# Optimization experiments

Measured on AMD Instinct MI355X. Metric: run time of the kernel, lower is better.

Reference implementation:

```python
import jax, jax.numpy as jnp
import numpy as np

D_MODEL = 1024
NUM_HEADS = 16
D_QK = D_MODEL // NUM_HEADS  # 64
SEQ_LEN = 4096
BATCH = 1
ROPE_THETA = 10000.0


def _apply_rope(x, positions):
    # x: [B, H, S, d], positions: [1, 1, S]
    d = x.shape[-1]
    inv_freq = 1.0 / (ROPE_THETA ** (jnp.arange(0, d, 2, dtype=jnp.float32) / d))  # [d/2]
    ang = positions.astype(jnp.float32)[..., None] * inv_freq  # [1,1,S,d/2]
    cos, sin = jnp.cos(ang), jnp.sin(ang)
    x1, x2 = x[..., 0::2], x[..., 1::2]
    out_even = x1 * cos - x2 * sin
    out_odd = x1 * sin + x2 * cos
    return jnp.stack([out_even, out_odd], axis=-1).reshape(x.shape)


def setup_inputs() -> dict:
    key = jax.random.key(0)
    ks = jax.random.split(key, 9)
    s = 1.0 / np.sqrt(D_MODEL)
    return {
        "x": jax.random.normal(ks[0], (BATCH, SEQ_LEN, D_MODEL), dtype=jnp.float32),
        "Wq": jax.random.normal(ks[1], (D_MODEL, D_MODEL), dtype=jnp.float32) * s,
        "bq": jnp.zeros((D_MODEL,), dtype=jnp.float32),
        "Wk": jax.random.normal(ks[2], (D_MODEL, D_MODEL), dtype=jnp.float32) * s,
        "bk": jnp.zeros((D_MODEL,), dtype=jnp.float32),
        "Wv": jax.random.normal(ks[3], (D_MODEL, D_MODEL), dtype=jnp.float32) * s,
        "bv": jnp.zeros((D_MODEL,), dtype=jnp.float32),
        "Wo": jax.random.normal(ks[4], (D_MODEL, D_MODEL), dtype=jnp.float32) * s,
        "bo": jnp.zeros((D_MODEL,), dtype=jnp.float32),
    }


def reference(x, Wq, bq, Wk, bk, Wv, bv, Wo, bo):
    B, S, D = x.shape
    H, dk = NUM_HEADS, D_QK
    positions = jnp.arange(S).reshape(1, 1, S)
    # torch Linear: x @ W.T + b. NOTE: original reshapes (B,S,H*dk) -> (B,H,S,dk)
    # without a transpose; we reproduce that exact (quirky) reshape.
    q = (x @ Wq.T + bq).reshape(B, H, S, dk)
    k = (x @ Wk.T + bk).reshape(B, H, S, dk)
    v = (x @ Wv.T + bv).reshape(B, H, S, dk)
    q = _apply_rope(q, positions)
    k = _apply_rope(k, positions)
    scores = jnp.einsum('bhqd,bhkd->bhqk', q, k) / jnp.sqrt(jnp.float32(dk))
    mask = jnp.tril(jnp.ones((S, S), dtype=bool))
    scores = jnp.where(mask, scores, -jnp.inf)
    attn = jax.nn.softmax(scores, axis=-1)
    out = jnp.einsum('bhqk,bhkd->bhqd', attn, v)  # [B,H,S,dk]
    concat = out.reshape(B, S, H * dk)  # mirrors original reshape back
    return concat @ Wo.T + bo
```

## Files before the change

kernel.cpp:

```cpp
#include <hip/hip_runtime.h>
#include <hip/hip_bf16.h>

typedef float f32x4 __attribute__((ext_vector_type(4)));
typedef __bf16 bf16x8 __attribute__((ext_vector_type(8)));
typedef short s16x4 __attribute__((ext_vector_type(4)));
typedef unsigned int u32;
typedef unsigned int u32x2 __attribute__((ext_vector_type(2)));
typedef unsigned short u16;

#define SEQ   4096
#define DM    1024
#define HEADS 16
#define DH    64

#if __has_builtin(__builtin_amdgcn_mfma_f32_16x16x16bf16_1k)
#define MFMA16_1K(A, B, C) __builtin_amdgcn_mfma_f32_16x16x16bf16_1k(A, B, C, 0, 0, 0)
#else
#define MFMA16_1K(A, B, C) (C)
#endif
#if __has_builtin(__builtin_amdgcn_exp2f)
#define FEXP2(x) __builtin_amdgcn_exp2f(x)
#else
#define FEXP2(x) exp2f(x)
#endif

__device__ __forceinline__ void async16(void* lds, const void* g) {
  __builtin_amdgcn_global_load_lds((const __attribute__((address_space(1))) u32*)g,
                                   (__attribute__((address_space(3))) u32*)lds, 16, 0, 0);
}

__device__ __forceinline__ u32 lds_addr(const void* p) {
  return (u32)(size_t)(const __attribute__((address_space(3))) char*)p;
}

__device__ __forceinline__ int swz(int row, int off) {
  return row * 128 + (off ^ ((((row >> 3) ^ row) & 7) << 4));
}

__device__ __forceinline__ float ubf2f(u32 u) {
  union { u32 x; float f; } c; c.x = u << 16; return c.f;
}
__device__ __forceinline__ u32 packbf(float a, float b) {
  __hip_bfloat16 ha = __float2bfloat16(a), hb = __float2bfloat16(b);
  return (u32)(*(u16*)&ha) | ((u32)(*(u16*)&hb) << 16);
}

__global__ __launch_bounds__(256) void prep_kernel(
    const float* __restrict__ x,  const float* __restrict__ Wq,
    const float* __restrict__ Wk, const float* __restrict__ Wv,
    const float* __restrict__ Wo, const float* __restrict__ bq,
    const float* __restrict__ bk, const float* __restrict__ bv,
    __hip_bfloat16* __restrict__ xb, __hip_bfloat16* __restrict__ Wqkv,
    __hip_bfloat16* __restrict__ Wob, float* __restrict__ bqkv)
{
  const int NX = SEQ * DM;
  const int NW = DM * DM;
  const int TOT = NX + 4 * NW + 3 * DM;
  for (int idx = blockIdx.x * 256 + threadIdx.x; idx < TOT; idx += gridDim.x * 256) {
    if (idx < NX) {
      xb[idx] = __float2bfloat16(x[idx]);
    } else if (idx < NX + 3 * NW) {
      int j = idx - NX; int m = j >> 20; int r = j & (NW - 1);
      const float* W = (m == 0) ? Wq : ((m == 1) ? Wk : Wv);
      Wqkv[j] = __float2bfloat16(W[r]);
    } else if (idx < NX + 4 * NW) {
      int r = idx - NX - 3 * NW;
      Wob[r] = __float2bfloat16(Wo[r]);
    } else {
      int r = idx - NX - 4 * NW;
      const float* b = (r < DM) ? bq : ((r < 2 * DM) ? bk : bv);
      bqkv[r] = b[r & (DM - 1)];
    }
  }
}

template<bool F32OUT>
__global__ __launch_bounds__(256) void gemm_bt(
    const __hip_bfloat16* __restrict__ A,
    const __hip_bfloat16* __restrict__ B,
    const float* __restrict__ bias,
    void* __restrict__ C,
    int M, int N, int K)
{
  __shared__ __hip_bfloat16 As[2][128 * 32];
  __shared__ __hip_bfloat16 Bs[2][128 * 32];
  const int tid = threadIdx.x;
  const int wid = tid >> 6, lane = tid & 63;
  const int l15 = lane & 15, l4 = lane >> 4;
  const int wr = wid >> 1, wc = wid & 1;
  const int lin = blockIdx.x;
  const int xcd = lin & 7, j = lin >> 3;
  const int bm = ((xcd << 2) | (j & 3)) * 128;
  const int bn = (j >> 2) * 128;

  f32x4 acc[4][4] = {};

  auto stage = [&](int buf, int k0) {
#pragma unroll
    for (int c = 0; c < 2; ++c) {
      int li = c * 256 + tid;
      const __hip_bfloat16* ga = A + (size_t)(bm + (li >> 2)) * K + k0 + (li & 3) * 8;
      async16((char*)(&As[buf][0]) + (c * 256 + wid * 64) * 16, ga);
    }
#pragma unroll
    for (int c = 0; c < 2; ++c) {
      int li = c * 256 + tid;
      const __hip_bfloat16* gb = B + (size_t)(bn + (li >> 2)) * K + k0 + (li & 3) * 8;
      async16((char*)(&Bs[buf][0]) + (c * 256 + wid * 64) * 16, gb);
    }
  };

  stage(0, 0);
  __syncthreads();
  const int nk = K >> 5;
  int cur = 0;
  for (int t = 0; t < nk; ++t) {
    if (t + 1 < nk) stage(cur ^ 1, (t + 1) << 5);
    bf16x8 af[4], bfr[4];
#pragma unroll
    for (int m = 0; m < 4; ++m)
      af[m] = *(const bf16x8*)(&As[cur][(wr * 64 + m * 16 + l15) * 32 + l4 * 8]);
#pragma unroll
    for (int n = 0; n < 4; ++n)
      bfr[n] = *(const bf16x8*)(&Bs[cur][(wc * 64 + n * 16 + l15) * 32 + l4 * 8]);
#pragma unroll
    for (int m = 0; m < 4; ++m)
#pragma unroll
      for (int n = 0; n < 4; ++n)
        acc[m][n] = __builtin_amdgcn_mfma_f32_16x16x32_bf16(af[m], bfr[n], acc[m][n], 0, 0, 0);
    __syncthreads();
    cur ^= 1;
  }

#pragma unroll
  for (int m = 0; m < 4; ++m) {
#pragma unroll
    for (int n = 0; n < 4; ++n) {
#pragma unroll
      for (int i = 0; i < 4; ++i) {
        int row = bm + wr * 64 + m * 16 + l4 * 4 + i;
        int col = bn + wc * 64 + n * 16 + l15;
        float v = acc[m][n][i] + bias[col];
        int mat = col >> 10;
        int cm = col & 1023;
        size_t oidx = ((size_t)mat << 22) + (size_t)row * DM + cm;
        if constexpr (F32OUT) ((float*)C)[oidx] = v;
        else ((__hip_bfloat16*)C)[oidx] = __float2bfloat16(v);
      }
    }
  }
}

__global__ __launch_bounds__(256) void gemm_bt64(
    const __hip_bfloat16* __restrict__ A,
    const __hip_bfloat16* __restrict__ B,
    const float* __restrict__ bias,
    float* __restrict__ C,
    int M, int N, int K)
{
  __shared__ __hip_bfloat16 As[2][64 * 32];
  __shared__ __hip_bfloat16 Bs[2][128 * 32];
  const int tid = threadIdx.x;
  const int wid = tid >> 6, lane = tid & 63;
  const int l15 = lane & 15, l4 = lane >> 4;
  const int lin = blockIdx.x;
  const int xcd = lin & 7, j = lin >> 3;
  const int bm = ((xcd << 3) | (j & 7)) * 64;
  const int bn = (j >> 3) * 128;

  f32x4 acc[4][2] = {};

  auto stage = [&](int buf, int k0) {
    {
      int li = tid;
      const __hip_bfloat16* ga = A + (size_t)(bm + (li >> 2)) * K + k0 + (li & 3) * 8;
      async16((char*)(&As[buf][0]) + (wid * 64) * 16, ga);
    }
#pragma unroll
    for (int c = 0; c < 2; ++c) {
      int li = c * 256 + tid;
      const __hip_bfloat16* gb = B + (size_t)(bn + (li >> 2)) * K + k0 + (li & 3) * 8;
      async16((char*)(&Bs[buf][0]) + (c * 256 + wid * 64) * 16, gb);
    }
  };

  stage(0, 0);
  __syncthreads();
  const int nk = K >> 5;
  int cur = 0;
  for (int t = 0; t < nk; ++t) {
    if (t + 1 < nk) stage(cur ^ 1, (t + 1) << 5);
    bf16x8 af[4], bfr[2];
#pragma unroll
    for (int m = 0; m < 4; ++m)
      af[m] = *(const bf16x8*)(&As[cur][(m * 16 + l15) * 32 + l4 * 8]);
#pragma unroll
    for (int n = 0; n < 2; ++n)
      bfr[n] = *(const bf16x8*)(&Bs[cur][(wid * 32 + n * 16 + l15) * 32 + l4 * 8]);
#pragma unroll
    for (int m = 0; m < 4; ++m)
#pragma unroll
      for (int n = 0; n < 2; ++n)
        acc[m][n] = __builtin_amdgcn_mfma_f32_16x16x32_bf16(af[m], bfr[n], acc[m][n], 0, 0, 0);
    __syncthreads();
    cur ^= 1;
  }

#pragma unroll
  for (int m = 0; m < 4; ++m) {
#pragma unroll
    for (int n = 0; n < 2; ++n) {
#pragma unroll
      for (int i = 0; i < 4; ++i) {
        int row = bm + m * 16 + l4 * 4 + i;
        int col = bn + wid * 32 + n * 16 + l15;
        C[(size_t)row * DM + col] = acc[m][n][i] + bias[col];
      }
    }
  }
}

__global__ __launch_bounds__(256) void rope_kernel(__hip_bfloat16* __restrict__ Q,
                                                   __hip_bfloat16* __restrict__ K)
{
  const int tid = blockIdx.x * 256 + threadIdx.x;
  const int i  = tid & 31;
  const int s2 = (tid >> 5) & (SEQ - 1);
  float inv = FEXP2(-0.41524101186092f * (float)i);
  float ang = (float)s2 * inv;
  float sn = __sinf(ang), cs = __cosf(ang);
  const float QS = 0.125f * 1.44269504088896f;
  size_t off = (size_t)tid * 2;
  u32 qw = *(u32*)(Q + off);
  float q1 = ubf2f(qw & 0xffffu), q2 = ubf2f(qw >> 16);
  *(u32*)(Q + off) = packbf((q1 * cs - q2 * sn) * QS, (q1 * sn + q2 * cs) * QS);
  u32 kw = *(u32*)(K + off);
  float k1 = ubf2f(kw & 0xffffu), k2 = ubf2f(kw >> 16);
  *(u32*)(K + off) = packbf(k1 * cs - k2 * sn, k1 * sn + k2 * cs);
}

__global__ __launch_bounds__(256) void attn_kernel(
    const __hip_bfloat16* __restrict__ Q,
    const __hip_bfloat16* __restrict__ K,
    const __hip_bfloat16* __restrict__ V,
    u16* __restrict__ Opart,
    float* __restrict__ lbuf)
{
  const int lin = blockIdx.x;
  const int pid  = (lin >> 4) & 31;
  const int half = (lin >> 3) & 1;
  const int h    = (lin & 7) | (((lin >> 9) & 1) << 3);
  const int tid = threadIdx.x, wid = tid >> 6, lane = tid & 63;
  const int l15 = lane & 15, l4 = lane >> 4;
  __shared__ __hip_bfloat16 Ks[2][64 * 64];
  __shared__ __hip_bfloat16 Vs[2][64 * 64];

  const size_t hbase = (size_t)h * SEQ * DH;
  const int qa = pid, qb = 63 - pid;
  const int a  = (pid >= 15) ? 16 : (31 - pid);
  const int t0 = half ? a : 0;
  const int t1 = half ? (64 - pid) : a;
  const int ra = qa * 64 + wid * 16, rb = qb * 64 + wid * 16;

  int goffK[2];
#pragma unroll
  for (int c = 0; c < 2; ++c) {
    int rowc = (wid * 2 + c) * 8 + (lane >> 3);
    int fc = ((wid * 2 + c) ^ (lane >> 3)) & 7;
    goffK[c] = rowc * DH + ((lane & 7) ^ fc) * 8;
  }
  int goffV[2];
#pragma unroll
  for (int c = 0; c < 2; ++c) {
    int s = (wid * 2 + c) * 2 + (lane >> 5);
    int g = s >> 2, n = s & 3;
    goffV[c] = (g * 16 + ((lane & 31) >> 1)) * DH + n * 16 + (lane & 1) * 8;
  }

  bf16x8 qfa[2], qfb[2];
#pragma unroll
  for (int dk = 0; dk < 2; ++dk) {
    qfa[dk] = *(const bf16x8*)(Q + hbase + (size_t)(ra + l15) * DH + dk * 32 + l4 * 8);
    qfb[dk] = *(const bf16x8*)(Q + hbase + (size_t)(rb + l15) * DH + dk * 32 + l4 * 8);
  }

  f32x4 oa[4] = {}, ob[4] = {};
  float la = 0.f, lb = 0.f;

  const u32 vsb0 = lds_addr(&Vs[0][0]) + (u32)(l15 * 8 + l4 * 128);
  const u32 vsb1 = vsb0 + 8192;

  auto stageK = [&](int buf, int tt) {
#pragma unroll
    for (int c = 0; c < 2; ++c)
      async16((char*)(&Ks[buf][0]) + (wid * 2 + c) * 1024,
              K + hbase + (size_t)tt * 64 * DH + goffK[c]);
  };
  auto stageV = [&](int buf, int tt) {
#pragma unroll
    for (int c = 0; c < 2; ++c)
      async16((char*)(&Vs[buf][0]) + (wid * 2 + c) * 1024,
              V + hbase + (size_t)tt * 64 * DH + goffV[c]);
  };

#define TRD(dst, base, imm) \
  asm volatile("ds_read_b64_tr_b16 %0, %1 offset:" #imm : "=v"(dst) : "v"(base))
#define CVTPK(d, a, b) \
  asm("v_cvt_pk_bf16_f32 %0, %1, %2" : "=v"(d) : "v"(a), "v"(b))
#define PV4(g) \
  { u32x2 wp_ = { w[g][0], w[g][1] }; \
    s16x4 pa_ = __builtin_bit_cast(s16x4, wp_); \
    _Pragma("unroll") \
    for (int n_ = 0; n_ < 4; ++n_) \
      oacc[n_] = MFMA16_1K(vr[g][n_], pa_, oacc[n_]); }

  auto frag = [&](int buf, int kb, bool diag, const bf16x8* qf, int r0,
                  float& l, f32x4* oacc) {
    const int myq = r0 + l15;
    f32x4 s[4];
#pragma unroll
    for (int g = 0; g < 4; ++g) {
      f32x4 z = {0.f, 0.f, 0.f, 0.f};
#pragma unroll
      for (int dk = 0; dk < 2; ++dk) {
        bf16x8 kf = *(const bf16x8*)((char*)(&Ks[buf][0]) +
                     swz(g * 16 + l15, dk * 64 + l4 * 16));
        z = __builtin_amdgcn_mfma_f32_16x16x32_bf16(kf, qf[dk], z, 0, 0, 0);
      }
      s[g] = z;
    }
    if (diag) {
#pragma unroll
      for (int g = 0; g < 4; ++g)
#pragma unroll
        for (int i = 0; i < 4; ++i)
          if (kb + g * 16 + l4 * 4 + i > myq) s[g][i] = -1e30f;
    }
#pragma unroll
    for (int g = 0; g < 4; ++g)
#pragma unroll
      for (int i = 0; i < 4; ++i) s[g][i] = FEXP2(s[g][i]);
    float rs = 0.f;
#pragma unroll
    for (int g = 0; g < 4; ++g)
      rs += (s[g][0] + s[g][1]) + (s[g][2] + s[g][3]);
    l += rs;
    u32 w[4][2];
#pragma unroll
    for (int g = 0; g < 4; ++g) {
      CVTPK(w[g][0], s[g][0], s[g][1]);
      CVTPK(w[g][1], s[g][2], s[g][3]);
    }
    const u32 va = buf ? vsb1 : vsb0;
    s16x4 vr[4][4];
    TRD(vr[0][0], va, 0);    TRD(vr[0][1], va, 512);
    TRD(vr[0][2], va, 1024); TRD(vr[0][3], va, 1536);
    TRD(vr[1][0], va, 2048); TRD(vr[1][1], va, 2560);
    TRD(vr[1][2], va, 3072); TRD(vr[1][3], va, 3584);
    asm volatile("s_waitcnt lgkmcnt(4)" ::: "memory");
    __builtin_amdgcn_sched_barrier(0);
    TRD(vr[2][0], va, 4096); TRD(vr[2][1], va, 4608);
    TRD(vr[2][2], va, 5120); TRD(vr[2][3], va, 5632);
    PV4(0)
    asm volatile("s_waitcnt lgkmcnt(4)" ::: "memory");
    __builtin_amdgcn_sched_barrier(0);
    TRD(vr[3][0], va, 6144); TRD(vr[3][1], va, 6656);
    TRD(vr[3][2], va, 7168); TRD(vr[3][3], va, 7680);
    PV4(1)
    asm volatile("s_waitcnt lgkmcnt(4)" ::: "memory");
    __builtin_amdgcn_sched_barrier(0);
    PV4(2)
    asm volatile("s_waitcnt lgkmcnt(0)" ::: "memory");
    __builtin_amdgcn_sched_barrier(0);
    PV4(3)
  };

  stageK(0, t0);
  stageV(0, t0);
  __syncthreads();

  for (int t = t0; t < t1; ++t) {
    const int cur = (t - t0) & 1, nxt = cur ^ 1;
    const bool pre = (t + 1 < t1);
    if (pre) { stageK(nxt, t + 1); stageV(nxt, t + 1); }
    frag(cur, t * 64, t == qb, qfb, rb, lb, ob);
    if (t <= qa) frag(cur, t * 64, t == qa, qfa, ra, la, oa);
    __syncthreads();
  }
#undef TRD
#undef CVTPK
#undef PV4

  la += __shfl_xor(la, 16); la += __shfl_xor(la, 32);
  lb += __shfl_xor(lb, 16); lb += __shfl_xor(lb, 32);
  auto write_partial = [&](int qt, float l, f32x4* oacc) {
    float rinv = (l > 0.f) ? 1.0f / l : 0.f;
    const int row = wid * 16 + l15;
    u16* po = Opart + ((((size_t)qt * HEADS + h) * 2 + half) * 64 + row) * 64;
#pragma unroll
    for (int n = 0; n < 4; ++n)
#pragma unroll
      for (int p = 0; p < 2; ++p)
        *(u32*)(po + n * 16 + l4 * 4 + 2 * p) =
            packbf(oacc[n][2 * p] * rinv, oacc[n][2 * p + 1] * rinv);
    if (l4 == 0)
      lbuf[((qt * HEADS + h) * 2 + half) * 64 + row] = l;
  };
  write_partial(qb, lb, ob);
  write_partial(qa, la, oa);
}

__global__ __launch_bounds__(256) void combine_kernel(
    const u16* __restrict__ Opart, const float* __restrict__ lbuf,
    __hip_bfloat16* __restrict__ concat)
{
  const int id = blockIdx.x * 256 + threadIdx.x;
  const int d0 = (id & 7) * 8;
  const int row = (id >> 3) & 63;
  const int h  = (id >> 9) & 15;
  const int qt = id >> 13;
  const int lb0 = ((qt * HEADS + h) * 2) * 64 + row;
  float w0 = lbuf[lb0], w1 = lbuf[lb0 + 64];
  float inv = 1.0f / (w0 + w1);
  w0 *= inv; w1 *= inv;
  size_t ob = (((size_t)(qt * HEADS + h) * 2) * 64 + row) * 64 + d0;
  uint4 a0 = *(const uint4*)(Opart + ob);
  uint4 a1 = *(const uint4*)(Opart + ob + 64 * 64);
  const u16* b0 = (const u16*)&a0; const u16* b1 = (const u16*)&a1;
  u32 outw[4];
#pragma unroll
  for (int j = 0; j < 4; ++j) {
    float e0 = ubf2f(b0[2 * j])     * w0 + ubf2f(b1[2 * j])     * w1;
    float e1 = ubf2f(b0[2 * j + 1]) * w0 + ubf2f(b1[2 * j + 1]) * w1;
    outw[j] = packbf(e0, e1);
  }
  *(uint4*)(concat + (size_t)h * SEQ * DH + (size_t)(qt * 64 + row) * DH + d0) =
      *(const uint4*)outw;
}

extern "C" void kernel_launch(void* const* d_in, const int* in_sizes, int n_in,
                              void* d_out, int out_size, void* d_ws, size_t ws_size,
                              hipStream_t stream) {
  (void)in_sizes; (void)n_in; (void)out_size; (void)ws_size;
  const float* x  = (const float*)d_in[0];
  const float* Wq = (const float*)d_in[1];
  const float* bq = (const float*)d_in[2];
  const float* Wk = (const float*)d_in[3];
  const float* bk = (const float*)d_in[4];
  const float* Wv = (const float*)d_in[5];
  const float* bv = (const float*)d_in[6];
  const float* Wo = (const float*)d_in[7];
  const float* bo = (const float*)d_in[8];

  char* ws = (char*)d_ws;
  __hip_bfloat16* Qbuf   = (__hip_bfloat16*)(ws + 0);
  __hip_bfloat16* Kbuf   = (__hip_bfloat16*)(ws + 8388608);
  __hip_bfloat16* Vbuf   = (__hip_bfloat16*)(ws + 16777216);
  __hip_bfloat16* concat = (__hip_bfloat16*)(ws + 25165824);
  __hip_bfloat16* Wob    = (__hip_bfloat16*)(ws + 33554432);
  float*          bqkv   = (float*)(ws + 35651584);
  float*          lbuf   = (float*)(ws + 35717120);
  __hip_bfloat16* xb     = (__hip_bfloat16*)(ws + 36765696);
  __hip_bfloat16* Wqkv   = (__hip_bfloat16*)(ws + 45154304);
  u16*            Opart  = (u16*)(ws + 36765696);

  prep_kernel<<<2048, 256, 0, stream>>>(x, Wq, Wk, Wv, Wo, bq, bk, bv, xb, Wqkv, Wob, bqkv);
  gemm_bt<false><<<768, 256, 0, stream>>>(xb, Wqkv, bqkv, (void*)Qbuf, SEQ, 3072, DM);
  rope_kernel<<<8192, 256, 0, stream>>>(Qbuf, Kbuf);
  attn_kernel<<<1024, 256, 0, stream>>>(Qbuf, Kbuf, Vbuf, Opart, lbuf);
  combine_kernel<<<2048, 256, 0, stream>>>(Opart, lbuf, concat);
  gemm_bt64<<<512, 256, 0, stream>>>(concat, Wob, bo, (float*)d_out, SEQ, DM, DM);
}
```

Measured before the change: 151.9 us.

## Fuse split-KV partial combine into output projection GEMM A-tile loading

Removes the separate combine kernel and instead merges the two attention partials (weighted by their softmax sums) while loading each A tile in the output-projection GEMM. The concat buffer's write and read round trip and one kernel launch go away. In exchange, the A loads become synchronous global loads with per-element arithmetic inside the GEMM main loop instead of async copies. Because the same A data is recombined for each of the 8 column-tile blocks, the combine arithmetic is repeated, and the loads may stall the pipeline.

```diff
diff --git a/kernel.cpp b/kernel.cpp
--- a/kernel.cpp
+++ b/kernel.cpp
@@ -151,8 +151,9 @@
   }
 }
 
-__global__ __launch_bounds__(256) void gemm_bt64(
-    const __hip_bfloat16* __restrict__ A,
+__global__ __launch_bounds__(256) void gemm_bt64_fused(
+    const u16* __restrict__ Opart,
+    const float* __restrict__ lbuf,
     const __hip_bfloat16* __restrict__ B,
     const float* __restrict__ bias,
     float* __restrict__ C,
@@ -168,14 +169,36 @@
   const int bm = ((xcd << 3) | (j & 7)) * 64;
   const int bn = (j >> 3) * 128;
 
+  const int arow = tid >> 2;
+  const int kloc = (tid & 3) * 8;
+
   f32x4 acc[4][2] = {};
 
-  auto stage = [&](int buf, int k0) {
-    {
-      int li = tid;
-      const __hip_bfloat16* ga = A + (size_t)(bm + (li >> 2)) * K + k0 + (li & 3) * 8;
-      async16((char*)(&As[buf][0]) + (wid * 64) * 16, ga);
-    }
+  auto stageA = [&](int buf, int k0) {
+    int kabs = k0 + kloc;
+    int r  = bm + arow;
+    int hh = r >> 8;
+    int s2 = ((r & 255) << 4) + (kabs >> 6);
+    int qq = s2 >> 6, orow = s2 & 63;
+    int dd = kabs & 63;
+    size_t base = ((((size_t)qq * HEADS + hh) * 2) * 64 + orow) * 64 + dd;
+    uint4 a0 = *(const uint4*)(Opart + base);
+    uint4 a1 = *(const uint4*)(Opart + base + 64 * 64);
+    int lb = ((qq * HEADS + hh) * 2) * 64 + orow;
+    float l0 = lbuf[lb], l1 = lbuf[lb + 64];
+    float inv = 1.0f / (l0 + l1);
+    float w0 = l0 * inv, w1 = l1 * inv;
+    const u16* b0 = (const u16*)&a0; const u16* b1 = (const u16*)&a1;
+    u32 outw[4];
+#pragma unroll
+    for (int p = 0; p < 4; ++p) {
+      float e0 = ubf2f(b0[2 * p])     * w0 + ubf2f(b1[2 * p])     * w1;
+      float e1 = ubf2f(b0[2 * p + 1]) * w0 + ubf2f(b1[2 * p + 1]) * w1;
+      outw[p] = packbf(e0, e1);
+    }
+    *(uint4*)(&As[buf][tid * 8]) = *(const uint4*)outw;
+  };
+  auto stageB = [&](int buf, int k0) {
 #pragma unroll
     for (int c = 0; c < 2; ++c) {
       int li = c * 256 + tid;
@@ -184,12 +207,13 @@
     }
   };
 
-  stage(0, 0);
+  stageA(0, 0);
+  stageB(0, 0);
   __syncthreads();
   const int nk = K >> 5;
   int cur = 0;
   for (int t = 0; t < nk; ++t) {
-    if (t + 1 < nk) stage(cur ^ 1, (t + 1) << 5);
+    if (t + 1 < nk) { stageB(cur ^ 1, (t + 1) << 5); stageA(cur ^ 1, (t + 1) << 5); }
     bf16x8 af[4], bfr[2];
 #pragma unroll
     for (int m = 0; m < 4; ++m)
@@ -410,34 +434,6 @@
   write_partial(qa, la, oa);
 }
 
-__global__ __launch_bounds__(256) void combine_kernel(
-    const u16* __restrict__ Opart, const float* __restrict__ lbuf,
-    __hip_bfloat16* __restrict__ concat)
-{
-  const int id = blockIdx.x * 256 + threadIdx.x;
-  const int d0 = (id & 7) * 8;
-  const int row = (id >> 3) & 63;
-  const int h  = (id >> 9) & 15;
-  const int qt = id >> 13;
-  const int lb0 = ((qt * HEADS + h) * 2) * 64 + row;
-  float w0 = lbuf[lb0], w1 = lbuf[lb0 + 64];
-  float inv = 1.0f / (w0 + w1);
-  w0 *= inv; w1 *= inv;
-  size_t ob = (((size_t)(qt * HEADS + h) * 2) * 64 + row) * 64 + d0;
-  uint4 a0 = *(const uint4*)(Opart + ob);
-  uint4 a1 = *(const uint4*)(Opart + ob + 64 * 64);
-  const u16* b0 = (const u16*)&a0; const u16* b1 = (const u16*)&a1;
-  u32 outw[4];
-#pragma unroll
-  for (int j = 0; j < 4; ++j) {
-    float e0 = ubf2f(b0[2 * j])     * w0 + ubf2f(b1[2 * j])     * w1;
-    float e1 = ubf2f(b0[2 * j + 1]) * w0 + ubf2f(b1[2 * j + 1]) * w1;
-    outw[j] = packbf(e0, e1);
-  }
-  *(uint4*)(concat + (size_t)h * SEQ * DH + (size_t)(qt * 64 + row) * DH + d0) =
-      *(const uint4*)outw;
-}
-
 extern "C" void kernel_launch(void* const* d_in, const int* in_sizes, int n_in,
                               void* d_out, int out_size, void* d_ws, size_t ws_size,
                               hipStream_t stream) {
@@ -456,7 +452,6 @@
   __hip_bfloat16* Qbuf   = (__hip_bfloat16*)(ws + 0);
   __hip_bfloat16* Kbuf   = (__hip_bfloat16*)(ws + 8388608);
   __hip_bfloat16* Vbuf   = (__hip_bfloat16*)(ws + 16777216);
-  __hip_bfloat16* concat = (__hip_bfloat16*)(ws + 25165824);
   __hip_bfloat16* Wob    = (__hip_bfloat16*)(ws + 33554432);
   float*          bqkv   = (float*)(ws + 35651584);
   float*          lbuf   = (float*)(ws + 35717120);
@@ -468,6 +463,5 @@
   gemm_bt<false><<<768, 256, 0, stream>>>(xb, Wqkv, bqkv, (void*)Qbuf, SEQ, 3072, DM);
   rope_kernel<<<8192, 256, 0, stream>>>(Qbuf, Kbuf);
   attn_kernel<<<1024, 256, 0, stream>>>(Qbuf, Kbuf, Vbuf, Opart, lbuf);
-  combine_kernel<<<2048, 256, 0, stream>>>(Opart, lbuf, concat);
-  gemm_bt64<<<512, 256, 0, stream>>>(concat, Wob, bo, (float*)d_out, SEQ, DM, DM);
-}
+  gemm_bt64_fused<<<512, 256, 0, stream>>>(Opart, lbuf, Wob, bo, (float*)d_out, SEQ, DM, DM);
+}
```

Measured after the change: 155.5 us. +2.4%, slower.
